# Kernel optimization log

Measured on AMD Instinct MI355X. Metric: run time of the kernel, lower is better.

Reference implementation:

```python
import jax, jax.numpy as jnp
import numpy as np

B, S, D, H = 4, 2048, 512, 4
HD = D // H
EPS = 1e-5


def layer_norm(x, gamma, beta):
    mu = jnp.mean(x, axis=-1, keepdims=True)
    var = jnp.mean(jnp.square(x - mu), axis=-1, keepdims=True)
    return (x - mu) * jax.lax.rsqrt(var + EPS) * gamma + beta


def setup_inputs() -> dict:
    key = jax.random.key(0)
    ks = jax.random.split(key, 16)
    s_in = 1.0 / np.sqrt(D)
    s_ex = 1.0 / np.sqrt(2 * D)
    return {
        "input_states": jax.random.normal(ks[0], (B, S, D), jnp.float32),
        "positions": jax.random.normal(ks[1], (B, S, 3), jnp.float32),
        "W_expand": jax.random.uniform(ks[2], (D, 2 * D), jnp.float32, -s_in, s_in),
        "b_expand": jax.random.uniform(ks[3], (2 * D,), jnp.float32, -s_in, s_in),
        "W_squeeze": jax.random.uniform(ks[4], (2 * D, D), jnp.float32, -s_ex, s_ex),
        "b_squeeze": jax.random.uniform(ks[5], (D,), jnp.float32, -s_ex, s_ex),
        "gamma": jnp.ones((D,), jnp.float32),
        "beta": jnp.zeros((D,), jnp.float32),
        "Wq": jax.random.uniform(ks[6], (D, D), jnp.float32, -s_in, s_in),
        "bq": jax.random.uniform(ks[7], (D,), jnp.float32, -s_in, s_in),
        "Wk": jax.random.uniform(ks[8], (D, D), jnp.float32, -s_in, s_in),
        "bk": jax.random.uniform(ks[9], (D,), jnp.float32, -s_in, s_in),
        "Wv": jax.random.uniform(ks[10], (D, D), jnp.float32, -s_in, s_in),
        "bv": jax.random.uniform(ks[11], (D,), jnp.float32, -s_in, s_in),
        "alpha": jnp.float32(0.1),
    }


def reference(input_states, positions, W_expand, b_expand, W_squeeze, b_squeeze,
              gamma, beta, Wq, bq, Wk, bk, Wv, bv, alpha):
    # FFN (expand -> relu -> squeeze) + residual + LayerNorm
    h = jax.nn.relu(input_states @ W_expand + b_expand)
    squeezed = h @ W_squeeze + b_squeeze
    se = layer_norm(input_states + squeezed, gamma, beta)

    # q/k/v projections, split heads: [B,H,S,HD]
    q = (se @ Wq + bq).reshape(B, S, H, HD).transpose(0, 2, 1, 3)
    k = (se @ Wk + bk).reshape(B, S, H, HD).transpose(0, 2, 1, 3)
    v = (se @ Wv + bv).reshape(B, S, H, HD).transpose(0, 2, 1, 3)

    scores = jnp.einsum('bhid,bhjd->bhij', q, k) / np.sqrt(HD)

    # squared pairwise distance bias: ||pi||^2 + ||pj||^2 - 2 pi.pj, broadcast over heads
    sq = jnp.sum(positions * positions, axis=-1)  # [B,S]
    dist2 = sq[:, :, None] + sq[:, None, :] - 2.0 * jnp.einsum('bic,bjc->bij', positions, positions)
    dist2 = jnp.maximum(dist2, 0.0)
    scores = scores - alpha * dist2[:, None, :, :]

    w = jax.nn.softmax(scores, axis=-1)
    ctx = jnp.einsum('bhij,bhjd->bhid', w, v)
    ctx = ctx.transpose(0, 2, 1, 3).reshape(B, S, D)

    # same LayerNorm params reused (self.norm applied twice in original)
    return layer_norm(se + ctx, gamma, beta)
```

## Files before the change

kernel.cpp:

```cpp
#include <hip/hip_runtime.h>

typedef __bf16 bf16_t;
typedef __attribute__((ext_vector_type(8))) __bf16 bf16x8;
typedef __attribute__((ext_vector_type(4))) __bf16 bf16x4;
typedef __attribute__((ext_vector_type(4))) float f32x4;
typedef __attribute__((ext_vector_type(16))) float f32x16;

constexpr int Bc = 4, Sc = 2048, Dc = 512, Hc = 4, HDc = 128;
constexpr int Mrows = Bc * Sc;

__device__ inline void gl2lds(const void* g, void* l) {
  __builtin_amdgcn_global_load_lds(
      (__attribute__((address_space(1))) void*)g,
      (__attribute__((address_space(3))) void*)l, 16, 0, 0);
}

__global__ __launch_bounds__(256) void prep_k(
    const float* __restrict__ X, bf16_t* __restrict__ xb,
    const float* __restrict__ We, bf16_t* __restrict__ wtE,
    const float* __restrict__ Ws, bf16_t* __restrict__ wtS,
    const float* __restrict__ Wq, const float* __restrict__ Wk,
    const float* __restrict__ Wv, bf16_t* __restrict__ wtQKV) {
  const int bid = blockIdx.x;
  if (bid < 2048) {
    const long i = ((long)bid * 256 + threadIdx.x) * 8;
    const float4 a = *(const float4*)(X + i);
    const float4 c = *(const float4*)(X + i + 4);
    bf16x8 o;
    o[0] = (bf16_t)a.x; o[1] = (bf16_t)a.y; o[2] = (bf16_t)a.z; o[3] = (bf16_t)a.w;
    o[4] = (bf16_t)c.x; o[5] = (bf16_t)c.y; o[6] = (bf16_t)c.z; o[7] = (bf16_t)c.w;
    *(bf16x8*)(xb + i) = o;
    return;
  }
  __shared__ float tile[32][33];
  const float* src; bf16_t* dst; int K, N, local;
  if (bid < 2560)      { src = We; dst = wtE; K = 512;  N = 1024; local = bid - 2048; }
  else if (bid < 3072) { src = Ws; dst = wtS; K = 1024; N = 512;  local = bid - 2560; }
  else if (bid < 3328) { src = Wq; dst = wtQKV;          K = 512; N = 512; local = bid - 3072; }
  else if (bid < 3584) { src = Wk; dst = wtQKV + 262144; K = 512; N = 512; local = bid - 3328; }
  else                 { src = Wv; dst = wtQKV + 524288; K = 512; N = 512; local = bid - 3584; }
  const int nb = N / 32;
  const int n0 = (local % nb) * 32, k0 = (local / nb) * 32;
  const int tx = threadIdx.x & 31, ty = threadIdx.x >> 5;
#pragma unroll
  for (int i = 0; i < 4; i++)
    tile[ty + i * 8][tx] = src[(long)(k0 + ty + i * 8) * N + n0 + tx];
  __syncthreads();
#pragma unroll
  for (int i = 0; i < 4; i++)
    dst[(long)(n0 + ty + i * 8) * K + k0 + tx] = (bf16_t)tile[tx][ty + i * 8];
}

__global__ __launch_bounds__(256) void pospack_k(const float* __restrict__ pos,
                                                 const float* __restrict__ alphap,
                                                 float* __restrict__ pos2) {
  const float aL = alphap[0] * 1.4426950408889634f;
  const int i = blockIdx.x * 256 + threadIdx.x;
  const float x = pos[(long)i * 3], y = pos[(long)i * 3 + 1], z = pos[(long)i * 3 + 2];
  float4 o; o.x = x; o.y = y; o.z = z; o.w = -aL * (x * x + y * y + z * z);
  *(float4*)(pos2 + (long)i * 4) = o;
}

template <int OMODE, int TN>
__global__ __launch_bounds__(256, (TN == 128) ? 2 : 3) void gemm128_k(
    const bf16_t* __restrict__ A, const bf16_t* __restrict__ Bt,
    const float* __restrict__ bias0, const float* __restrict__ bias1,
    const float* __restrict__ bias2, void* __restrict__ out0,
    void* __restrict__ out1, void* __restrict__ out2, int N, int K) {
  __shared__ bf16_t As[2][128 * 64];
  __shared__ bf16_t Bs[2][TN * 64];
  constexpr int MT = (TN == 128) ? 4 : 2;
  constexpr int BI = (TN == 128) ? 4 : 2;
  constexpr int MW = (TN == 128) ? 64 : 32;
  const int t = threadIdx.x;
  const int n0 = blockIdx.x * TN, m0 = blockIdx.y * 128;
  const int lane = t & 63, wave = t >> 6;
  const int quad = lane >> 4, ln = lane & 15;
  const int wm = (TN == 128) ? (wave >> 1) : wave;
  const int wn = (TN == 128) ? (wave & 1) : 0;
  const int l8 = lane >> 3, g = lane & 7;
  const bf16_t* aseg = A + (long)(m0 + wave * 32 + l8) * K + (g ^ l8) * 8;
  const bf16_t* bseg = Bt + (long)(n0 + wave * (BI * 8) + l8) * K + (g ^ l8) * 8;
  auto stage = [&](int buf, int k0) {
#pragma unroll
    for (int i = 0; i < 4; i++)
      gl2lds(aseg + (long)i * 8 * K + k0, &As[buf][(wave * 32 + i * 8) * 64]);
#pragma unroll
    for (int i = 0; i < BI; i++)
      gl2lds(bseg + (long)i * 8 * K + k0, &Bs[buf][(wave * BI * 8 + i * 8) * 64]);
  };
  f32x4 acc[MT][4] = {};
  stage(0, 0);
  const int niter = K / 64;
  for (int it = 0; it < niter; it++) {
    const int cur = it & 1;
    __syncthreads();
    if (it + 1 < niter) stage(1 - cur, (it + 1) * 64);
#pragma unroll
    for (int kc = 0; kc < 2; kc++) {
      bf16x8 af[MT], bfr[4];
#pragma unroll
      for (int mt = 0; mt < MT; mt++)
        af[mt] = *(const bf16x8*)&As[cur][(wm * MW + mt * 16 + ln) * 64 +
                                          (((kc * 4 + quad) ^ (ln & 7)) * 8)];
#pragma unroll
      for (int nt = 0; nt < 4; nt++)
        bfr[nt] = *(const bf16x8*)&Bs[cur][(wn * 64 + nt * 16 + ln) * 64 +
                                           (((kc * 4 + quad) ^ (ln & 7)) * 8)];
#pragma unroll
      for (int mt = 0; mt < MT; mt++)
#pragma unroll
        for (int nt = 0; nt < 4; nt++)
          acc[mt][nt] = __builtin_amdgcn_mfma_f32_16x16x32_bf16(af[mt], bfr[nt],
                                                                acc[mt][nt], 0, 0, 0);
    }
  }
#pragma unroll
  for (int nt = 0; nt < 4; nt++) {
    const int gcol = n0 + wn * 64 + nt * 16 + ln;
    if constexpr (OMODE == 0 || OMODE == 1) {
      const float bv = bias0[gcol];
      bf16_t* o = (bf16_t*)out0;
#pragma unroll
      for (int mt = 0; mt < MT; mt++)
#pragma unroll
        for (int r = 0; r < 4; r++) {
          const int grow = m0 + wm * MW + mt * 16 + quad * 4 + r;
          float vv = acc[mt][nt][r] + bv;
          if constexpr (OMODE == 0) vv = vv > 0.f ? vv : 0.f;
          o[(long)grow * N + gcol] = (bf16_t)vv;
        }
    } else {
      const int which = gcol >> 9, n = gcol & 511;
      const int hh = n >> 7, hd = n & 127;
      const float bv = (which == 0 ? bias0 : which == 1 ? bias1 : bias2)[n];
      bf16_t* o = (bf16_t*)(which == 0 ? out0 : which == 1 ? out1 : out2);
#pragma unroll
      for (int mt = 0; mt < MT; mt++)
#pragma unroll
        for (int r = 0; r < 4; r++) {
          const int grow = m0 + wm * MW + mt * 16 + quad * 4 + r;
          const int b = grow >> 11, s = grow & 2047;
          const float vv = acc[mt][nt][r] + bv;
          long idx;
          if (which == 0) {
            idx = ((long)((b * Hc + hh) * Sc + s)) * HDc + hd;
          } else if (which == 1) {
            const int tt = s >> 6, kh = (s >> 5) & 1, key = s & 31;
            const int c = hd >> 4, lk = key + 32 * ((hd >> 3) & 1), j = hd & 7;
            idx = ((((long)((b * Hc + hh) * 32 + tt) * 2 + kh) * 8 + c) * 64 + lk) * 8 + j;
          } else {
            const int tt = s >> 6, ht2 = hd >> 5, kc = (s & 63) >> 4;
            const int lk = (hd & 31) + 32 * ((s >> 3) & 1), j = s & 7;
            idx = ((((long)((b * Hc + hh) * 32 + tt) * 4 + ht2) * 4 + kc) * 64 + lk) * 8 + j;
          }
          o[idx] = (bf16_t)vv;
        }
    }
  }
}

template <int DUAL>
__global__ __launch_bounds__(256) void ln_k(const float* __restrict__ xa,
                                            const bf16_t* __restrict__ xb,
                                            const float* __restrict__ gamma,
                                            const float* __restrict__ beta,
                                            float* __restrict__ out,
                                            bf16_t* __restrict__ outb) {
  const int wave = threadIdx.x >> 6, lane = threadIdx.x & 63;
  const long row = (long)blockIdx.x * 4 + wave;
  const float* a = xa + row * Dc;
  const bf16_t* bp = xb + row * Dc;
  float vv[8];
  float s = 0.f, s2 = 0.f;
#pragma unroll
  for (int i = 0; i < 2; i++) {
    const float4 va = *(const float4*)(a + lane * 4 + i * 256);
    const bf16x4 vb = *(const bf16x4*)(bp + lane * 4 + i * 256);
    const float xs[4] = {va.x, va.y, va.z, va.w};
#pragma unroll
    for (int j = 0; j < 4; j++) {
      const float x = xs[j] + (float)vb[j];
      vv[i * 4 + j] = x;
      s += x;
      s2 += x * x;
    }
  }
#pragma unroll
  for (int off = 1; off < 64; off <<= 1) {
    s += __shfl_xor(s, off, 64);
    s2 += __shfl_xor(s2, off, 64);
  }
  const float mu = s * (1.f / Dc);
  const float var = s2 * (1.f / Dc) - mu * mu;
  const float rstd = rsqrtf(var + 1e-5f);
#pragma unroll
  for (int i = 0; i < 2; i++)
#pragma unroll
    for (int j = 0; j < 4; j++) {
      const int col = lane * 4 + i * 256 + j;
      const float o = (vv[i * 4 + j] - mu) * rstd * gamma[col] + beta[col];
      out[row * Dc + col] = o;
      if constexpr (DUAL) outb[row * Dc + col] = (bf16_t)o;
    }
}

__global__ __launch_bounds__(256, 2) void attn_k(const bf16_t* __restrict__ q,
                                                 const bf16_t* __restrict__ Kg,
                                                 const bf16_t* __restrict__ Vg,
                                                 const float* __restrict__ pos2,
                                                 const float* __restrict__ alphap,
                                                 bf16_t* __restrict__ ctx) {
  __shared__ bf16_t Ks[2][8192];
  __shared__ bf16_t Vts[2][8192];
  __shared__ float pk4[2][64][4];
  __shared__ bf16_t Ps[4][1024];
  __shared__ float RsD[4][32];
  const int t = threadIdx.x;
  const int qt = blockIdx.x, h = blockIdx.y, b = blockIdx.z;
  const int q0 = qt * 64;
  const int wave = t >> 6, lane = t & 63;
  const int l31 = lane & 31, hb = lane >> 5;
  const int rh = wave & 1, kh = wave >> 1;
  const float l2e = 1.4426950408889634f;
  const float scale_l2 = l2e * 0.08838834764831845f;
  const float aL = alphap[0] * l2e;

  bf16x8 qf[8];
  const long qrow = (long)((b * Hc + h) * Sc + q0 + rh * 32 + l31);
#pragma unroll
  for (int c = 0; c < 8; c++)
    qf[c] = *(const bf16x8*)(q + qrow * HDc + c * 16 + hb * 8);
  float pqx, pqy, pqz;
  {
    const float4 p = *(const float4*)(pos2 + (long)(b * Sc + q0 + rh * 32 + l31) * 4);
    pqx = 2.f * aL * p.x; pqy = 2.f * aL * p.y; pqz = 2.f * aL * p.z;
  }

  const bf16_t* ktile = Kg + (long)((b * Hc + h) * 32) * 8192 + lane * 8;
  const bf16_t* vtile = Vg + (long)((b * Hc + h) * 32) * 8192 + lane * 8;
  const float* pcur = pos2 + (long)b * Sc * 4 + lane * 4;
  auto stage = [&](int buf) {
#pragma unroll
    for (int i = 0; i < 4; i++)
      gl2lds(ktile + (wave * 4 + i) * 512, &Ks[buf][(wave * 4 + i) * 512]);
#pragma unroll
    for (int i = 0; i < 4; i++)
      gl2lds(vtile + (wave * 4 + i) * 512, &Vts[buf][(wave * 4 + i) * 512]);
    if (wave == 0) gl2lds(pcur, &pk4[buf][0][0]);
  };
  stage(0);
  ktile += 8192; vtile += 8192; pcur += 256;

  float rsl = 0.f;
  f32x16 accT[4] = {};
  bf16_t* pwbase = &Ps[wave][l31 * 8 + 4 * hb];

  for (int kt = 0; kt < Sc / 64; kt++) {
    const int cur = kt & 1;
    __syncthreads();
    if (kt < Sc / 64 - 1) {
      stage(1 - cur);
      ktile += 8192; vtile += 8192; pcur += 256;
    }
    f32x16 sacc = {};
#pragma unroll
    for (int c = 0; c < 8; c++) {
      const bf16x8 kf = *(const bf16x8*)&Ks[cur][(kh * 8 + c) * 512 + lane * 8];
      sacc = __builtin_amdgcn_mfma_f32_32x32x16_bf16(kf, qf[c], sacc, 0, 0, 0);
    }
#pragma unroll
    for (int g2 = 0; g2 < 4; g2++)
#pragma unroll
      for (int r0 = 0; r0 < 4; r0++) {
        const int kp = r0 + 4 * hb + 8 * g2;
        const float4 pv = *(const float4*)&pk4[cur][kh * 32 + kp][0];
        const float bias = __builtin_fmaf(pqx, pv.x,
                           __builtin_fmaf(pqy, pv.y,
                           __builtin_fmaf(pqz, pv.z, pv.w)));
        const float p = __builtin_amdgcn_exp2f(
            __builtin_fmaf(sacc[g2 * 4 + r0], scale_l2, bias));
        rsl += p;
        pwbase[(g2 >> 1) * 512 + (g2 & 1) * 256 + r0] = (bf16_t)p;
      }
    const bf16x8 pf0 = *(const bf16x8*)&Ps[wave][lane * 8];
    const bf16x8 pf1 = *(const bf16x8*)&Ps[wave][512 + lane * 8];
#pragma unroll
    for (int ht = 0; ht < 4; ht++) {
      const bf16x8 v0 = *(const bf16x8*)&Vts[cur][(ht * 4 + kh * 2 + 0) * 512 + lane * 8];
      accT[ht] = __builtin_amdgcn_mfma_f32_32x32x16_bf16(v0, pf0, accT[ht], 0, 0, 0);
      const bf16x8 v1 = *(const bf16x8*)&Vts[cur][(ht * 4 + kh * 2 + 1) * 512 + lane * 8];
      accT[ht] = __builtin_amdgcn_mfma_f32_32x32x16_bf16(v1, pf1, accT[ht], 0, 0, 0);
    }
  }
  __syncthreads();

  rsl += __shfl_xor(rsl, 32, 64);
  if (hb == 0) RsD[wave][l31] = rsl;
  float* Oc = (float*)&Ks[0][0];
  if (kh == 1) {
#pragma unroll
    for (int ht = 0; ht < 4; ht++)
#pragma unroll
      for (int r = 0; r < 16; r++) {
        const int hdp = (r & 3) + 8 * (r >> 2) + 4 * hb;
        Oc[(ht * 32 + hdp) * 64 + rh * 32 + l31] = accT[ht][r];
      }
  }
  __syncthreads();
  if (kh == 0) {
    const float rinv = 1.f / (RsD[wave][l31] + RsD[wave + 2][l31]);
    const long orow = (long)(b * Sc + q0 + rh * 32 + l31);
#pragma unroll
    for (int ht = 0; ht < 4; ht++)
#pragma unroll
      for (int g2 = 0; g2 < 4; g2++) {
        bf16x4 ov;
#pragma unroll
        for (int r0 = 0; r0 < 4; r0++) {
          const int hdp = r0 + 8 * g2 + 4 * hb;
          ov[r0] = (bf16_t)((accT[ht][g2 * 4 + r0] +
                             Oc[(ht * 32 + hdp) * 64 + rh * 32 + l31]) * rinv);
        }
        *(bf16x4*)(ctx + orow * Dc + h * HDc + ht * 32 + 8 * g2 + 4 * hb) = ov;
      }
  }
}

constexpr size_t SE_OFF = 0;
constexpr size_t SQB_OFF = 16777216;
constexpr size_t SEB_OFF = 25165824;
constexpr size_t Q_OFF = 33554432;
constexpr size_t K_OFF = 41943040;
constexpr size_t V_OFF = 50331648;
constexpr size_t XB_OFF = Q_OFF;
constexpr size_t H_OFF = K_OFF;
constexpr size_t POS2_OFF = SEB_OFF;
constexpr size_t WTE_OFF = 58720256;
constexpr size_t WTS_OFF = WTE_OFF + 1048576;
constexpr size_t WTQKV_OFF = WTS_OFF + 1048576;

extern "C" void kernel_launch(void* const* d_in, const int* in_sizes, int n_in,
                              void* d_out, int out_size, void* d_ws, size_t ws_size,
                              hipStream_t stream) {
  const float* X = (const float*)d_in[0];
  const float* pos = (const float*)d_in[1];
  const float* W_expand = (const float*)d_in[2];
  const float* b_expand = (const float*)d_in[3];
  const float* W_squeeze = (const float*)d_in[4];
  const float* b_squeeze = (const float*)d_in[5];
  const float* gamma = (const float*)d_in[6];
  const float* beta = (const float*)d_in[7];
  const float* Wq = (const float*)d_in[8];
  const float* bq = (const float*)d_in[9];
  const float* Wk = (const float*)d_in[10];
  const float* bk = (const float*)d_in[11];
  const float* Wv = (const float*)d_in[12];
  const float* bv = (const float*)d_in[13];
  const float* alphap = (const float*)d_in[14];

  char* ws = (char*)d_ws;
  float* se = (float*)(ws + SE_OFF);
  bf16_t* sqb = (bf16_t*)(ws + SQB_OFF);
  bf16_t* ctxb = (bf16_t*)(ws + SQB_OFF);
  bf16_t* seb = (bf16_t*)(ws + SEB_OFF);
  float* pos2 = (float*)(ws + POS2_OFF);
  bf16_t* qb = (bf16_t*)(ws + Q_OFF);
  bf16_t* kb = (bf16_t*)(ws + K_OFF);
  bf16_t* vb = (bf16_t*)(ws + V_OFF);
  bf16_t* xbb = (bf16_t*)(ws + XB_OFF);
  bf16_t* hb = (bf16_t*)(ws + H_OFF);
  bf16_t* wtE = (bf16_t*)(ws + WTE_OFF);
  bf16_t* wtS = (bf16_t*)(ws + WTS_OFF);
  bf16_t* wtQKV = (bf16_t*)(ws + WTQKV_OFF);

  prep_k<<<3840, 256, 0, stream>>>(X, xbb, W_expand, wtE, W_squeeze, wtS,
                                   Wq, Wk, Wv, wtQKV);
  gemm128_k<0, 128><<<dim3(1024 / 128, Mrows / 128), 256, 0, stream>>>(
      xbb, wtE, b_expand, nullptr, nullptr, hb, nullptr, nullptr, 1024, 512);
  gemm128_k<1, 64><<<dim3(512 / 64, Mrows / 128), 256, 0, stream>>>(
      hb, wtS, b_squeeze, nullptr, nullptr, sqb, nullptr, nullptr, 512, 1024);
  ln_k<1><<<Mrows / 4, 256, 0, stream>>>(X, sqb, gamma, beta, se, seb);
  gemm128_k<2, 128><<<dim3(1536 / 128, Mrows / 128), 256, 0, stream>>>(
      seb, wtQKV, bq, bk, bv, qb, kb, vb, 1536, 512);
  pospack_k<<<Mrows / 256, 256, 0, stream>>>(pos, alphap, pos2);
  attn_k<<<dim3(Sc / 64, Hc, Bc), 256, 0, stream>>>(qb, kb, vb, pos2, alphap, ctxb);
  ln_k<0><<<Mrows / 4, 256, 0, stream>>>(se, ctxb, gamma, beta, (float*)d_out, nullptr);

  (void)in_sizes; (void)n_in; (void)out_size; (void)ws_size;
}
```

Before: 233.5 us.

## Fold pospack into prep, swizzle block order, vectorize LayerNorm, drop fp32 se

Several changes land together. The position packing moves into the prep kernel, which removes one launch. The GEMM and attention grids become 1D with a swizzled block-to-tile mapping meant to improve L2/XCD locality. LayerNorm now loads and stores 8 contiguous elements per lane and reads gamma and beta as vectors. The fp32 `se` buffer is dropped, so the second LayerNorm reads the bf16 `seb` for the residual, which cuts memory traffic but lowers the precision of the residual path. Attention also packs its probability writes to LDS into bf16x4 stores.

```diff
diff --git a/kernel.cpp b/kernel.cpp
--- a/kernel.cpp
+++ b/kernel.cpp
@@ -17,6 +17,8 @@
 
 __global__ __launch_bounds__(256) void prep_k(
     const float* __restrict__ X, bf16_t* __restrict__ xb,
+    const float* __restrict__ pos, const float* __restrict__ alphap,
+    float* __restrict__ pos2,
     const float* __restrict__ We, bf16_t* __restrict__ wtE,
     const float* __restrict__ Ws, bf16_t* __restrict__ wtS,
     const float* __restrict__ Wq, const float* __restrict__ Wk,
@@ -32,13 +34,21 @@
     *(bf16x8*)(xb + i) = o;
     return;
   }
+  if (bid < 2080) {
+    const float aL = alphap[0] * 1.4426950408889634f;
+    const int i = (bid - 2048) * 256 + threadIdx.x;
+    const float x = pos[(long)i * 3], y = pos[(long)i * 3 + 1], z = pos[(long)i * 3 + 2];
+    float4 o; o.x = x; o.y = y; o.z = z; o.w = -aL * (x * x + y * y + z * z);
+    *(float4*)(pos2 + (long)i * 4) = o;
+    return;
+  }
   __shared__ float tile[32][33];
   const float* src; bf16_t* dst; int K, N, local;
-  if (bid < 2560)      { src = We; dst = wtE; K = 512;  N = 1024; local = bid - 2048; }
-  else if (bid < 3072) { src = Ws; dst = wtS; K = 1024; N = 512;  local = bid - 2560; }
-  else if (bid < 3328) { src = Wq; dst = wtQKV;          K = 512; N = 512; local = bid - 3072; }
-  else if (bid < 3584) { src = Wk; dst = wtQKV + 262144; K = 512; N = 512; local = bid - 3328; }
-  else                 { src = Wv; dst = wtQKV + 524288; K = 512; N = 512; local = bid - 3584; }
+  if (bid < 2592)      { src = We; dst = wtE; K = 512;  N = 1024; local = bid - 2080; }
+  else if (bid < 3104) { src = Ws; dst = wtS; K = 1024; N = 512;  local = bid - 2592; }
+  else if (bid < 3360) { src = Wq; dst = wtQKV;          K = 512; N = 512; local = bid - 3104; }
+  else if (bid < 3616) { src = Wk; dst = wtQKV + 262144; K = 512; N = 512; local = bid - 3360; }
+  else                 { src = Wv; dst = wtQKV + 524288; K = 512; N = 512; local = bid - 3616; }
   const int nb = N / 32;
   const int n0 = (local % nb) * 32, k0 = (local / nb) * 32;
   const int tx = threadIdx.x & 31, ty = threadIdx.x >> 5;
@@ -51,17 +61,7 @@
     dst[(long)(n0 + ty + i * 8) * K + k0 + tx] = (bf16_t)tile[tx][ty + i * 8];
 }
 
-__global__ __launch_bounds__(256) void pospack_k(const float* __restrict__ pos,
-                                                 const float* __restrict__ alphap,
-                                                 float* __restrict__ pos2) {
-  const float aL = alphap[0] * 1.4426950408889634f;
-  const int i = blockIdx.x * 256 + threadIdx.x;
-  const float x = pos[(long)i * 3], y = pos[(long)i * 3 + 1], z = pos[(long)i * 3 + 2];
-  float4 o; o.x = x; o.y = y; o.z = z; o.w = -aL * (x * x + y * y + z * z);
-  *(float4*)(pos2 + (long)i * 4) = o;
-}
-
-template <int OMODE, int TN>
+template <int OMODE, int TN, int NB>
 __global__ __launch_bounds__(256, (TN == 128) ? 2 : 3) void gemm128_k(
     const bf16_t* __restrict__ A, const bf16_t* __restrict__ Bt,
     const float* __restrict__ bias0, const float* __restrict__ bias1,
@@ -73,7 +73,11 @@
   constexpr int BI = (TN == 128) ? 4 : 2;
   constexpr int MW = (TN == 128) ? 64 : 32;
   const int t = threadIdx.x;
-  const int n0 = blockIdx.x * TN, m0 = blockIdx.y * 128;
+  const int p = blockIdx.x;
+  const int slot = p >> 3;
+  const int by = (p & 7) + 8 * (slot / NB);
+  const int bx = slot % NB;
+  const int n0 = bx * TN, m0 = by * 128;
   const int lane = t & 63, wave = t >> 6;
   const int quad = lane >> 4, ln = lane & 15;
   const int wm = (TN == 128) ? (wave >> 1) : wave;
@@ -160,32 +164,32 @@
   }
 }
 
-template <int DUAL>
-__global__ __launch_bounds__(256) void ln_k(const float* __restrict__ xa,
+template <int AF32, int OF32>
+__global__ __launch_bounds__(256) void ln_k(const void* __restrict__ xa,
                                             const bf16_t* __restrict__ xb,
                                             const float* __restrict__ gamma,
                                             const float* __restrict__ beta,
-                                            float* __restrict__ out,
-                                            bf16_t* __restrict__ outb) {
+                                            void* __restrict__ out) {
   const int wave = threadIdx.x >> 6, lane = threadIdx.x & 63;
   const long row = (long)blockIdx.x * 4 + wave;
-  const float* a = xa + row * Dc;
-  const bf16_t* bp = xb + row * Dc;
+  const int col0 = lane * 8;
   float vv[8];
   float s = 0.f, s2 = 0.f;
-#pragma unroll
-  for (int i = 0; i < 2; i++) {
-    const float4 va = *(const float4*)(a + lane * 4 + i * 256);
-    const bf16x4 vb = *(const bf16x4*)(bp + lane * 4 + i * 256);
-    const float xs[4] = {va.x, va.y, va.z, va.w};
-#pragma unroll
-    for (int j = 0; j < 4; j++) {
-      const float x = xs[j] + (float)vb[j];
-      vv[i * 4 + j] = x;
-      s += x;
-      s2 += x * x;
-    }
-  }
+  const bf16x8 vb = *(const bf16x8*)(xb + row * Dc + col0);
+  if constexpr (AF32) {
+    const float* a = (const float*)xa + row * Dc + col0;
+    const float4 a0 = *(const float4*)a;
+    const float4 a1 = *(const float4*)(a + 4);
+    const float xs[8] = {a0.x, a0.y, a0.z, a0.w, a1.x, a1.y, a1.z, a1.w};
+#pragma unroll
+    for (int j = 0; j < 8; j++) vv[j] = xs[j] + (float)vb[j];
+  } else {
+    const bf16x8 va = *(const bf16x8*)((const bf16_t*)xa + row * Dc + col0);
+#pragma unroll
+    for (int j = 0; j < 8; j++) vv[j] = (float)va[j] + (float)vb[j];
+  }
+#pragma unroll
+  for (int j = 0; j < 8; j++) { s += vv[j]; s2 += vv[j] * vv[j]; }
 #pragma unroll
   for (int off = 1; off < 64; off <<= 1) {
     s += __shfl_xor(s, off, 64);
@@ -194,15 +198,30 @@
   const float mu = s * (1.f / Dc);
   const float var = s2 * (1.f / Dc) - mu * mu;
   const float rstd = rsqrtf(var + 1e-5f);
-#pragma unroll
-  for (int i = 0; i < 2; i++)
-#pragma unroll
-    for (int j = 0; j < 4; j++) {
-      const int col = lane * 4 + i * 256 + j;
-      const float o = (vv[i * 4 + j] - mu) * rstd * gamma[col] + beta[col];
-      out[row * Dc + col] = o;
-      if constexpr (DUAL) outb[row * Dc + col] = (bf16_t)o;
-    }
+  const float4 g0 = *(const float4*)(gamma + col0);
+  const float4 g1 = *(const float4*)(gamma + col0 + 4);
+  const float4 b0 = *(const float4*)(beta + col0);
+  const float4 b1 = *(const float4*)(beta + col0 + 4);
+  const float gs[8] = {g0.x, g0.y, g0.z, g0.w, g1.x, g1.y, g1.z, g1.w};
+  const float bs[8] = {b0.x, b0.y, b0.z, b0.w, b1.x, b1.y, b1.z, b1.w};
+  if constexpr (OF32) {
+    float* o = (float*)out + row * Dc + col0;
+    float4 o0, o1;
+    o0.x = (vv[0] - mu) * rstd * gs[0] + bs[0];
+    o0.y = (vv[1] - mu) * rstd * gs[1] + bs[1];
+    o0.z = (vv[2] - mu) * rstd * gs[2] + bs[2];
+    o0.w = (vv[3] - mu) * rstd * gs[3] + bs[3];
+    o1.x = (vv[4] - mu) * rstd * gs[4] + bs[4];
+    o1.y = (vv[5] - mu) * rstd * gs[5] + bs[5];
+    o1.z = (vv[6] - mu) * rstd * gs[6] + bs[6];
+    o1.w = (vv[7] - mu) * rstd * gs[7] + bs[7];
+    *(float4*)o = o0; *(float4*)(o + 4) = o1;
+  } else {
+    bf16x8 ob;
+#pragma unroll
+    for (int j = 0; j < 8; j++) ob[j] = (bf16_t)((vv[j] - mu) * rstd * gs[j] + bs[j]);
+    *(bf16x8*)((bf16_t*)out + row * Dc + col0) = ob;
+  }
 }
 
 __global__ __launch_bounds__(256, 2) void attn_k(const bf16_t* __restrict__ q,
@@ -217,7 +236,10 @@
   __shared__ bf16_t Ps[4][1024];
   __shared__ float RsD[4][32];
   const int t = threadIdx.x;
-  const int qt = blockIdx.x, h = blockIdx.y, b = blockIdx.z;
+  const int p = blockIdx.x;
+  const int qt = (p >> 3) & 31;
+  const int gg = (p & 7) + 8 * (p >> 8);
+  const int h = gg & 3, b = gg >> 2;
   const int q0 = qt * 64;
   const int wave = t >> 6, lane = t & 63;
   const int l31 = lane & 31, hb = lane >> 5;
@@ -233,8 +255,8 @@
     qf[c] = *(const bf16x8*)(q + qrow * HDc + c * 16 + hb * 8);
   float pqx, pqy, pqz;
   {
-    const float4 p = *(const float4*)(pos2 + (long)(b * Sc + q0 + rh * 32 + l31) * 4);
-    pqx = 2.f * aL * p.x; pqy = 2.f * aL * p.y; pqz = 2.f * aL * p.z;
+    const float4 pv = *(const float4*)(pos2 + (long)(b * Sc + q0 + rh * 32 + l31) * 4);
+    pqx = 2.f * aL * pv.x; pqy = 2.f * aL * pv.y; pqz = 2.f * aL * pv.z;
   }
 
   const bf16_t* ktile = Kg + (long)((b * Hc + h) * 32) * 8192 + lane * 8;
@@ -270,7 +292,8 @@
       sacc = __builtin_amdgcn_mfma_f32_32x32x16_bf16(kf, qf[c], sacc, 0, 0, 0);
     }
 #pragma unroll
-    for (int g2 = 0; g2 < 4; g2++)
+    for (int g2 = 0; g2 < 4; g2++) {
+      bf16x4 pq4;
 #pragma unroll
       for (int r0 = 0; r0 < 4; r0++) {
         const int kp = r0 + 4 * hb + 8 * g2;
@@ -278,11 +301,13 @@
         const float bias = __builtin_fmaf(pqx, pv.x,
                            __builtin_fmaf(pqy, pv.y,
                            __builtin_fmaf(pqz, pv.z, pv.w)));
-        const float p = __builtin_amdgcn_exp2f(
+        const float pe = __builtin_amdgcn_exp2f(
             __builtin_fmaf(sacc[g2 * 4 + r0], scale_l2, bias));
-        rsl += p;
-        pwbase[(g2 >> 1) * 512 + (g2 & 1) * 256 + r0] = (bf16_t)p;
+        rsl += pe;
+        pq4[r0] = (bf16_t)pe;
       }
+      *(bf16x4*)(pwbase + (g2 >> 1) * 512 + (g2 & 1) * 256) = pq4;
+    }
     const bf16x8 pf0 = *(const bf16x8*)&Ps[wave][lane * 8];
     const bf16x8 pf1 = *(const bf16x8*)&Ps[wave][512 + lane * 8];
 #pragma unroll
@@ -327,16 +352,15 @@
   }
 }
 
-constexpr size_t SE_OFF = 0;
-constexpr size_t SQB_OFF = 16777216;
-constexpr size_t SEB_OFF = 25165824;
-constexpr size_t Q_OFF = 33554432;
-constexpr size_t K_OFF = 41943040;
-constexpr size_t V_OFF = 50331648;
+constexpr size_t SQB_OFF = 0;
+constexpr size_t SEB_OFF = 8388608;
+constexpr size_t Q_OFF = 16777216;
+constexpr size_t K_OFF = 25165824;
+constexpr size_t V_OFF = 33554432;
 constexpr size_t XB_OFF = Q_OFF;
 constexpr size_t H_OFF = K_OFF;
-constexpr size_t POS2_OFF = SEB_OFF;
-constexpr size_t WTE_OFF = 58720256;
+constexpr size_t POS2_OFF = 41943040;
+constexpr size_t WTE_OFF = POS2_OFF + 131072;
 constexpr size_t WTS_OFF = WTE_OFF + 1048576;
 constexpr size_t WTQKV_OFF = WTS_OFF + 1048576;
 
@@ -360,7 +384,6 @@
   const float* alphap = (const float*)d_in[14];
 
   char* ws = (char*)d_ws;
-  float* se = (float*)(ws + SE_OFF);
   bf16_t* sqb = (bf16_t*)(ws + SQB_OFF);
   bf16_t* ctxb = (bf16_t*)(ws + SQB_OFF);
   bf16_t* seb = (bf16_t*)(ws + SEB_OFF);
@@ -374,18 +397,17 @@
   bf16_t* wtS = (bf16_t*)(ws + WTS_OFF);
   bf16_t* wtQKV = (bf16_t*)(ws + WTQKV_OFF);
 
-  prep_k<<<3840, 256, 0, stream>>>(X, xbb, W_expand, wtE, W_squeeze, wtS,
-                                   Wq, Wk, Wv, wtQKV);
-  gemm128_k<0, 128><<<dim3(1024 / 128, Mrows / 128), 256, 0, stream>>>(
+  prep_k<<<3872, 256, 0, stream>>>(X, xbb, pos, alphap, pos2,
+                                   W_expand, wtE, W_squeeze, wtS, Wq, Wk, Wv, wtQKV);
+  gemm128_k<0, 128, 8><<<512, 256, 0, stream>>>(
       xbb, wtE, b_expand, nullptr, nullptr, hb, nullptr, nullptr, 1024, 512);
-  gemm128_k<1, 64><<<dim3(512 / 64, Mrows / 128), 256, 0, stream>>>(
+  gemm128_k<1, 64, 8><<<512, 256, 0, stream>>>(
       hb, wtS, b_squeeze, nullptr, nullptr, sqb, nullptr, nullptr, 512, 1024);
-  ln_k<1><<<Mrows / 4, 256, 0, stream>>>(X, sqb, gamma, beta, se, seb);
-  gemm128_k<2, 128><<<dim3(1536 / 128, Mrows / 128), 256, 0, stream>>>(
+  ln_k<1, 0><<<Mrows / 4, 256, 0, stream>>>(X, sqb, gamma, beta, seb);
+  gemm128_k<2, 128, 12><<<768, 256, 0, stream>>>(
       seb, wtQKV, bq, bk, bv, qb, kb, vb, 1536, 512);
-  pospack_k<<<Mrows / 256, 256, 0, stream>>>(pos, alphap, pos2);
-  attn_k<<<dim3(Sc / 64, Hc, Bc), 256, 0, stream>>>(qb, kb, vb, pos2, alphap, ctxb);
-  ln_k<0><<<Mrows / 4, 256, 0, stream>>>(se, ctxb, gamma, beta, (float*)d_out, nullptr);
+  attn_k<<<512, 256, 0, stream>>>(qb, kb, vb, pos2, alphap, ctxb);
+  ln_k<0, 1><<<Mrows / 4, 256, 0, stream>>>(seb, ctxb, gamma, beta, (float*)d_out);
 
   (void)in_sizes; (void)n_in; (void)out_size; (void)ws_size;
 }
```

Result: faster. 222.2 us (-4.9%).
